# Kernel optimization log

Hardware: AMD Instinct MI355X
Metric: run time of the kernel (lower is better)

Reference implementation:

```python
import jax, jax.numpy as jnp
import numpy as np

# STBLISModule forward. Original torch code materializes kron(s_wav, t_wav)
# [K*J, N*T, N*T] and contracts: filtered[b,c,d,nt] = sum_k kron[d,nt,k] x[b,c,k].
# Since kron(S_p, T_q)[n*T+t, m*T+u] = S_p[n,m] * T_q[t,u] (row-major flatten),
# this equals the separable form y[b,c,p,q] = S_p @ X[b,c] @ T_q^T, which we
# compute directly (identical math, no giant dense kron matrix).

B, C, N, T = 4, 4, 512, 256
K, J = 4, 4


def setup_inputs() -> dict:
    key = jax.random.key(0)
    k1, k2, k3 = jax.random.split(key, 3)
    x = jax.random.normal(k1, (B, C, N, T), dtype=jnp.float32)
    s_wav = jax.random.normal(k2, (K, N, N), dtype=jnp.float32)  # spatial wavelet bank
    t_wav = jax.random.normal(k3, (J, T, T), dtype=jnp.float32)  # temporal wavelet bank
    return {"x": x, "s_wav": s_wav, "t_wav": t_wav}


def reference(x, s_wav, t_wav):
    # spatial filtering: [B,C,K,N,T]
    tmp = jnp.einsum('pnm,bcmu->bcpnu', s_wav, x)
    # temporal filtering: [B,C,K,J,N,T]; note sum over last axis u of t_wav
    # matches kron/einsum 'ijk,mlk' contraction (i.e. X @ T_q^T)
    y = jnp.einsum('bcpnu,qtu->bcpqnt', tmp, t_wav)
    b, c, p, q, n, t = y.shape
    # D index ordering d = p*J + q matches torch.kron filter ordering
    y = y.reshape(b, c * p * q, n, t)
    # dual ReLU split, concatenated on channel dim
    return jnp.concatenate([jax.nn.relu(y), jax.nn.relu(-y)], axis=1)
```

## Files before the change

kernel.cpp:

```cpp
#include <hip/hip_runtime.h>
#include <hip/hip_bf16.h>

typedef __attribute__((ext_vector_type(8))) short bf16x8;
typedef __attribute__((ext_vector_type(4))) float f32x4;
typedef __attribute__((ext_vector_type(4))) int   i32x4;
typedef __attribute__((ext_vector_type(2))) int   i32x2;

#define DEV static __device__ __forceinline__

DEV unsigned short f2bf(float f) {
  __hip_bfloat16 h = __float2bfloat16(f);
  return __builtin_bit_cast(unsigned short, h);
}
DEV int pack2(float a, float b) {
  return (int)f2bf(a) | ((int)f2bf(b) << 16);
}
DEV bf16x8 ldsFrag(const char* p, int off) {
  i32x4 v = *(const i32x4*)(p + off);
  return __builtin_bit_cast(bf16x8, v);
}


__global__ __launch_bounds__(256) void cvt_all(
    const float* __restrict__ x, unsigned short* __restrict__ xt,
    const float* __restrict__ sw, unsigned short* __restrict__ swb,
    const float* __restrict__ tw, unsigned short* __restrict__ twb)
{
  const int bid = blockIdx.x;
  const int tid = threadIdx.x;
  if (bid < 512) {
    __shared__ unsigned short lt[64][72];
    const int ut = bid & 3;
    const int mt = (bid >> 2) & 7;
    const int bc = bid >> 5;
    const int ul = tid & 63;
    const int mr = tid >> 6;
    const float* px = x + ((size_t)bc * 512 + mt * 64) * 256 + ut * 64;
#pragma unroll
    for (int r = 0; r < 16; r++) {
      int m = r * 4 + mr;
      lt[m][ul] = f2bf(px[(size_t)m * 256 + ul]);
    }
    __syncthreads();
    const int t8 = tid >> 5;
    const int a  = t8 & 3;
    const int bb = t8 >> 2;
    const int l0 = tid & 31;
    unsigned short* tilep =
        xt + (((size_t)(bc * 16 + ut * 4 + a)) * 16 + (mt * 2 + bb)) * 512;
#pragma unroll
    for (int h = 0; h < 2; h++) {
      int l = l0 + h * 32;
      int ur = a * 16 + (l & 15);
      int mb = bb * 32 + (l >> 4) * 8;
      i32x4 w;
#pragma unroll
      for (int j = 0; j < 4; j++)
        w[j] = (int)lt[mb + 2 * j][ur] | ((int)lt[mb + 2 * j + 1][ur] << 16);
      *(i32x4*)(tilep + l * 8) = w;
    }
  } else if (bid < 1024) {
    const int tile = (bid - 512) * 4 + (tid >> 6);
    const int l = tid & 63;
    const int mt2 = tile & 15;
    const int nt2 = (tile >> 4) & 31;
    const int p   = tile >> 9;
    const float* ps = sw + ((size_t)p * 512 + nt2 * 16 + (l & 15)) * 512
                         + mt2 * 32 + (l >> 4) * 8;
    f32x4 A = ((const f32x4*)ps)[0], Bv = ((const f32x4*)ps)[1];
    i32x4 w;
    w[0] = pack2(A[0], A[1]);  w[1] = pack2(A[2], A[3]);
    w[2] = pack2(Bv[0], Bv[1]); w[3] = pack2(Bv[2], Bv[3]);
    *(i32x4*)(swb + (size_t)tile * 512 + l * 8) = w;
  } else {
    const int tile = (bid - 1024) * 4 + (tid >> 6);
    const int l = tid & 63;
    const int ut2 = tile & 7;
    const int tt2 = (tile >> 3) & 15;
    const int q   = tile >> 7;
    const float* pt = tw + ((size_t)q * 256 + tt2 * 16 + (l & 15)) * 256
                         + ut2 * 32 + (l >> 4) * 8;
    f32x4 A = ((const f32x4*)pt)[0], Bv = ((const f32x4*)pt)[1];
    i32x4 w;
    w[0] = pack2(A[0], A[1]);  w[1] = pack2(A[2], A[3]);
    w[2] = pack2(Bv[0], Bv[1]); w[3] = pack2(Bv[2], Bv[3]);
    *(i32x4*)(twb + (size_t)tile * 512 + l * 8) = w;
  }
}

__global__ __launch_bounds__(512, 4) void stblis_main(
    const unsigned short* __restrict__ xt, const unsigned short* __restrict__ swb,
    const unsigned short* __restrict__ twb, float* __restrict__ out)
{
  __shared__ __align__(16) char lds[65536];
  char* const tmp = lds;
  char* const stg = lds + 32768;

  const int tid  = threadIdx.x;
  const int lane = tid & 63;
  const int wid  = tid >> 6;
  const int l15  = lane & 15;
  const int l4   = lane >> 4;

  const int bx = blockIdx.x;
  const int nt = bx & 7;
  const int p  = (bx >> 3) & 3;
  const int bc = bx >> 5;
  const int n0 = nt * 64;
  const int b = bc >> 2, c = bc & 3;

  const int wu = wid >> 1;
  const int wn = wid & 1;

  f32x4 acc[4][2];
#pragma unroll
  for (int i = 0; i < 4; i++)
#pragma unroll
    for (int j = 0; j < 2; j++) acc[i][j] = {0.f, 0.f, 0.f, 0.f};

  const unsigned short* xA = xt  + (((size_t)(bc * 16 + wu * 4)) * 16) * 512 + lane * 8;
  const unsigned short* sB = swb + (((size_t)(p * 32 + nt * 4 + wn * 2)) * 16) * 512 + lane * 8;

  for (int kc = 0; kc < 8; kc++) {
#pragma unroll
    for (int ks = 0; ks < 2; ks++) {
      const int mt2 = kc * 2 + ks;
      bf16x8 af[4], bg[2];
#pragma unroll
      for (int uf = 0; uf < 4; uf++)
        af[uf] = *(const bf16x8*)(xA + ((size_t)uf * 16 + mt2) * 512);
#pragma unroll
      for (int nf = 0; nf < 2; nf++)
        bg[nf] = *(const bf16x8*)(sB + ((size_t)nf * 16 + mt2) * 512);
#pragma unroll
      for (int uf = 0; uf < 4; uf++)
#pragma unroll
        for (int nf = 0; nf < 2; nf++)
          acc[uf][nf] = __builtin_amdgcn_mfma_f32_16x16x32_bf16(
              af[uf], bg[nf], acc[uf][nf], 0, 0, 0);
    }
  }

#pragma unroll
  for (int uf = 0; uf < 4; uf++)
#pragma unroll
    for (int nf = 0; nf < 2; nf++) {
      int u0 = wu * 64 + uf * 16 + l4 * 4;
      int n  = wn * 32 + nf * 16 + l15;
      i32x2 w;
      w[0] = pack2(acc[uf][nf][0], acc[uf][nf][1]);
      w[1] = pack2(acc[uf][nf][2], acc[uf][nf][3]);
      *(i32x2*)(tmp + n * 512 + (((u0 >> 3) ^ (n & 7)) << 4) + (u0 & 7) * 2) = w;
    }
  __syncthreads();

  const int tq = wid >> 1;
  const int nh = wid & 1;
  const int rowA = nh * 32 + l15;
  const int rowB = nh * 32 + 16 + l15;

  bf16x8 bgA[8], bgB[8];

#define LOADBG(dst, ph16)                                                      \
  {                                                                            \
    const int q_ = (ph16) >> 2, tc_ = (ph16) & 3;                              \
    const unsigned short* tA_ =                                                \
        twb + (((size_t)(q_ * 16 + tc_ * 4 + tq)) * 8) * 512 + lane * 8;       \
    _Pragma("unroll")                                                          \
    for (int us_ = 0; us_ < 8; us_++)                                          \
      dst[us_] = *(const bf16x8*)(tA_ + (size_t)us_ * 512);                    \
  }

#define SUB(cur, tcl)                                                          \
  {                                                                            \
    f32x4 a20 = {0.f, 0.f, 0.f, 0.f};                                          \
    f32x4 a21 = {0.f, 0.f, 0.f, 0.f};                                          \
    _Pragma("unroll")                                                          \
    for (int us_ = 0; us_ < 8; us_++) {                                        \
      const int slot_ = (us_ * 4 + l4) ^ (l15 & 7);                            \
      bf16x8 af0_ = ldsFrag(tmp, rowA * 512 + (slot_ << 4));                   \
      bf16x8 af1_ = ldsFrag(tmp, rowB * 512 + (slot_ << 4));                   \
      a20 = __builtin_amdgcn_mfma_f32_16x16x32_bf16(cur[us_], af0_, a20, 0, 0, 0); \
      a21 = __builtin_amdgcn_mfma_f32_16x16x32_bf16(cur[us_], af1_, a21, 0, 0, 0); \
    }                                                                          \
    const int c32_ = (tcl) * 16 + tq * 4 + l4;                                 \
    *(f32x4*)(stg + rowA * 512 + ((c32_ ^ (rowA & 15)) << 4)) = a20;           \
    *(f32x4*)(stg + rowB * 512 + ((c32_ ^ (rowB & 15)) << 4)) = a21;           \
  }

  LOADBG(bgA, 0);

  for (int ph = 0; ph < 8; ph++) {
    const int q  = ph >> 1;
    const int th = ph & 1;

    if (ph) asm volatile("s_barrier" ::: "memory");

    LOADBG(bgB, 2 * ph + 1);
    SUB(bgA, 0);
    if (ph < 7) LOADBG(bgA, 2 * ph + 2);
    SUB(bgB, 1);

    asm volatile("s_waitcnt lgkmcnt(0)\n\ts_barrier" ::: "memory");

    float* outQP = out + ((size_t)(b * 128 + c * 16 + p * 4 + q) * 512 + n0) * 256;
    float* outQN = outQP + (size_t)64 * 512 * 256;
#pragma unroll
    for (int it = 0; it < 4; it++) {
      int g   = it * 512 + tid;
      int r   = g >> 5;
      int c32 = g & 31;
      f32x4 y = *(const f32x4*)(stg + r * 512 + ((c32 ^ (r & 15)) << 4));
      f32x4 vP, vN;
#pragma unroll
      for (int j = 0; j < 4; j++) {
        vP[j] = fmaxf(y[j], 0.f);
        vN[j] = fmaxf(-y[j], 0.f);
      }
      size_t go = (size_t)r * 256 + th * 128 + c32 * 4;
      *(f32x4*)(outQP + go) = vP;
      *(f32x4*)(outQN + go) = vN;
    }
  }
#undef SUB
#undef LOADBG
}

extern "C" void kernel_launch(void* const* d_in, const int* in_sizes, int n_in,
                              void* d_out, int out_size, void* d_ws, size_t ws_size,
                              hipStream_t stream) {
  (void)in_sizes; (void)n_in; (void)out_size; (void)ws_size;
  const float* x  = (const float*)d_in[0];
  const float* sw = (const float*)d_in[1];
  const float* tw = (const float*)d_in[2];
  float* out = (float*)d_out;

  unsigned short* xt  = (unsigned short*)d_ws;
  unsigned short* swb = xt + (size_t)16 * 16 * 16 * 512;
  unsigned short* twb = swb + (size_t)2048 * 512;

  cvt_all<<<dim3(1152), dim3(256), 0, stream>>>(x, xt, sw, swb, tw, twb);
  stblis_main<<<dim3(512), dim3(512), 0, stream>>>(xt, swb, twb, out);
}
```

Before: 74.17 us.

## Process two spatial tiles per block, overlapping second stage-1 GEMM with first stage-2

```diff
diff --git a/kernel.cpp b/kernel.cpp
--- a/kernel.cpp
+++ b/kernel.cpp
@@ -88,13 +88,14 @@
   }
 }
 
-__global__ __launch_bounds__(512, 4) void stblis_main(
+__global__ __launch_bounds__(512, 2) void stblis_main(
     const unsigned short* __restrict__ xt, const unsigned short* __restrict__ swb,
     const unsigned short* __restrict__ twb, float* __restrict__ out)
 {
-  __shared__ __align__(16) char lds[65536];
-  char* const tmp = lds;
-  char* const stg = lds + 32768;
+  __shared__ __align__(16) char lds[131072];
+  char* const tmp0 = lds;
+  char* const tmp1 = lds + 32768;
+  char* const stgb = lds + 65536;
 
   const int tid  = threadIdx.x;
   const int lane = tid & 63;
@@ -102,24 +103,25 @@
   const int l15  = lane & 15;
   const int l4   = lane >> 4;
 
-  const int bx = blockIdx.x;
-  const int nt = bx & 7;
-  const int p  = (bx >> 3) & 3;
-  const int bc = bx >> 5;
-  const int n0 = nt * 64;
+  const int bx  = blockIdx.x;
+  const int ntp = bx & 3;
+  const int p   = (bx >> 2) & 3;
+  const int bc  = bx >> 4;
+  const int nt0 = ntp * 2, nt1 = ntp * 2 + 1;
   const int b = bc >> 2, c = bc & 3;
 
   const int wu = wid >> 1;
   const int wn = wid & 1;
 
+  const unsigned short* xA  = xt  + (((size_t)(bc * 16 + wu * 4)) * 16) * 512 + lane * 8;
+  const unsigned short* sB0 = swb + (((size_t)(p * 32 + nt0 * 4 + wn * 2)) * 16) * 512 + lane * 8;
+  const unsigned short* sB1 = swb + (((size_t)(p * 32 + nt1 * 4 + wn * 2)) * 16) * 512 + lane * 8;
+
   f32x4 acc[4][2];
 #pragma unroll
   for (int i = 0; i < 4; i++)
 #pragma unroll
     for (int j = 0; j < 2; j++) acc[i][j] = {0.f, 0.f, 0.f, 0.f};
-
-  const unsigned short* xA = xt  + (((size_t)(bc * 16 + wu * 4)) * 16) * 512 + lane * 8;
-  const unsigned short* sB = swb + (((size_t)(p * 32 + nt * 4 + wn * 2)) * 16) * 512 + lane * 8;
 
   for (int kc = 0; kc < 8; kc++) {
 #pragma unroll
@@ -131,7 +133,7 @@
         af[uf] = *(const bf16x8*)(xA + ((size_t)uf * 16 + mt2) * 512);
 #pragma unroll
       for (int nf = 0; nf < 2; nf++)
-        bg[nf] = *(const bf16x8*)(sB + ((size_t)nf * 16 + mt2) * 512);
+        bg[nf] = *(const bf16x8*)(sB0 + ((size_t)nf * 16 + mt2) * 512);
 #pragma unroll
       for (int uf = 0; uf < 4; uf++)
 #pragma unroll
@@ -140,7 +142,6 @@
               af[uf], bg[nf], acc[uf][nf], 0, 0, 0);
     }
   }
-
 #pragma unroll
   for (int uf = 0; uf < 4; uf++)
 #pragma unroll
@@ -150,14 +151,17 @@
       i32x2 w;
       w[0] = pack2(acc[uf][nf][0], acc[uf][nf][1]);
       w[1] = pack2(acc[uf][nf][2], acc[uf][nf][3]);
-      *(i32x2*)(tmp + n * 512 + (((u0 >> 3) ^ (n & 7)) << 4) + (u0 & 7) * 2) = w;
+      *(i32x2*)(tmp0 + n * 512 + (((u0 >> 3) ^ (n & 7)) << 4) + (u0 & 7) * 2) = w;
     }
   __syncthreads();
 
   const int tq = wid >> 1;
   const int nh = wid & 1;
   const int rowA = nh * 32 + l15;
-  const int rowB = nh * 32 + 16 + l15;
+  const int rowB = rowA + 16;
+
+  float* const outB0 = out + (((size_t)(b * 128 + c * 16 + p * 4)) * 512 + nt0 * 64) * 256;
+  float* const outB1 = out + (((size_t)(b * 128 + c * 16 + p * 4)) * 512 + nt1 * 64) * 256;
 
   bf16x8 bgA[8], bgB[8];
 
@@ -171,59 +175,125 @@
       dst[us_] = *(const bf16x8*)(tA_ + (size_t)us_ * 512);                    \
   }
 
-#define SUB(cur, tcl)                                                          \
+#define SUB(tmpP, stgP, cur, tcl)                                              \
   {                                                                            \
     f32x4 a20 = {0.f, 0.f, 0.f, 0.f};                                          \
     f32x4 a21 = {0.f, 0.f, 0.f, 0.f};                                          \
     _Pragma("unroll")                                                          \
     for (int us_ = 0; us_ < 8; us_++) {                                        \
       const int slot_ = (us_ * 4 + l4) ^ (l15 & 7);                            \
-      bf16x8 af0_ = ldsFrag(tmp, rowA * 512 + (slot_ << 4));                   \
-      bf16x8 af1_ = ldsFrag(tmp, rowB * 512 + (slot_ << 4));                   \
+      bf16x8 af0_ = ldsFrag(tmpP, rowA * 512 + (slot_ << 4));                  \
+      bf16x8 af1_ = ldsFrag(tmpP, rowB * 512 + (slot_ << 4));                  \
       a20 = __builtin_amdgcn_mfma_f32_16x16x32_bf16(cur[us_], af0_, a20, 0, 0, 0); \
       a21 = __builtin_amdgcn_mfma_f32_16x16x32_bf16(cur[us_], af1_, a21, 0, 0, 0); \
     }                                                                          \
     const int c32_ = (tcl) * 16 + tq * 4 + l4;                                 \
-    *(f32x4*)(stg + rowA * 512 + ((c32_ ^ (rowA & 15)) << 4)) = a20;           \
-    *(f32x4*)(stg + rowB * 512 + ((c32_ ^ (rowB & 15)) << 4)) = a21;           \
-  }
+    *(f32x4*)(stgP + rowA * 512 + ((c32_ ^ (rowA & 15)) << 4)) = a20;          \
+    *(f32x4*)(stgP + rowB * 512 + ((c32_ ^ (rowB & 15)) << 4)) = a21;          \
+  }
+
+#define STOREPH(stgR, outBase, qv, thv)                                        \
+  {                                                                            \
+    float* oP_ = (outBase) + (size_t)(qv) * 131072;                            \
+    float* oN_ = oP_ + 8388608;                                                \
+    _Pragma("unroll")                                                          \
+    for (int it_ = 0; it_ < 4; it_++) {                                        \
+      int g_ = it_ * 512 + tid;                                                \
+      int r_ = g_ >> 5;                                                        \
+      int c32_ = g_ & 31;                                                      \
+      f32x4 y_ = *(const f32x4*)(stgR + r_ * 512 + ((c32_ ^ (r_ & 15)) << 4)); \
+      f32x4 vP_, vN_;                                                          \
+      _Pragma("unroll")                                                        \
+      for (int j_ = 0; j_ < 4; j_++) {                                         \
+        vP_[j_] = fmaxf(y_[j_], 0.f);                                          \
+        vN_[j_] = fmaxf(-y_[j_], 0.f);                                         \
+      }                                                                        \
+      size_t go_ = (size_t)r_ * 256 + (thv) * 128 + c32_ * 4;                  \
+      *(f32x4*)(oP_ + go_) = vP_;                                              \
+      *(f32x4*)(oN_ + go_) = vN_;                                              \
+    }                                                                          \
+  }
+
+#define LOADA1(K, F0, F1, F2, F3, G0, G1)                                      \
+  {                                                                            \
+    const int mt2_ = (K);                                                      \
+    F0 = *(const bf16x8*)(xA + ((size_t)0 * 16 + mt2_) * 512);                 \
+    F1 = *(const bf16x8*)(xA + ((size_t)1 * 16 + mt2_) * 512);                 \
+    F2 = *(const bf16x8*)(xA + ((size_t)2 * 16 + mt2_) * 512);                 \
+    F3 = *(const bf16x8*)(xA + ((size_t)3 * 16 + mt2_) * 512);                 \
+    G0 = *(const bf16x8*)(sB1 + ((size_t)0 * 16 + mt2_) * 512);                \
+    G1 = *(const bf16x8*)(sB1 + ((size_t)1 * 16 + mt2_) * 512);                \
+  }
+
+#define MFMA1K(F0, F1, F2, F3, G0, G1)                                         \
+  c1_00 = __builtin_amdgcn_mfma_f32_16x16x32_bf16(F0, G0, c1_00, 0, 0, 0);     \
+  c1_01 = __builtin_amdgcn_mfma_f32_16x16x32_bf16(F0, G1, c1_01, 0, 0, 0);     \
+  c1_10 = __builtin_amdgcn_mfma_f32_16x16x32_bf16(F1, G0, c1_10, 0, 0, 0);     \
+  c1_11 = __builtin_amdgcn_mfma_f32_16x16x32_bf16(F1, G1, c1_11, 0, 0, 0);     \
+  c1_20 = __builtin_amdgcn_mfma_f32_16x16x32_bf16(F2, G0, c1_20, 0, 0, 0);     \
+  c1_21 = __builtin_amdgcn_mfma_f32_16x16x32_bf16(F2, G1, c1_21, 0, 0, 0);     \
+  c1_30 = __builtin_amdgcn_mfma_f32_16x16x32_bf16(F3, G0, c1_30, 0, 0, 0);     \
+  c1_31 = __builtin_amdgcn_mfma_f32_16x16x32_bf16(F3, G1, c1_31, 0, 0, 0);
+
+#define WT1(ACC, UF, NF)                                                       \
+  {                                                                            \
+    int u0_ = wu * 64 + (UF) * 16 + l4 * 4;                                    \
+    int n_  = wn * 32 + (NF) * 16 + l15;                                       \
+    i32x2 w_;                                                                  \
+    w_[0] = pack2(ACC[0], ACC[1]);                                             \
+    w_[1] = pack2(ACC[2], ACC[3]);                                             \
+    *(i32x2*)(tmp1 + n_ * 512 + (((u0_ >> 3) ^ (n_ & 7)) << 4) + (u0_ & 7) * 2) = w_; \
+  }
+
+  f32x4 c1_00 = {0.f,0.f,0.f,0.f}, c1_01 = {0.f,0.f,0.f,0.f};
+  f32x4 c1_10 = {0.f,0.f,0.f,0.f}, c1_11 = {0.f,0.f,0.f,0.f};
+  f32x4 c1_20 = {0.f,0.f,0.f,0.f}, c1_21 = {0.f,0.f,0.f,0.f};
+  f32x4 c1_30 = {0.f,0.f,0.f,0.f}, c1_31 = {0.f,0.f,0.f,0.f};
+  bf16x8 k0f0, k0f1, k0f2, k0f3, k0g0, k0g1;
+  bf16x8 k1f0, k1f1, k1f2, k1f3, k1g0, k1g1;
 
   LOADBG(bgA, 0);
 
   for (int ph = 0; ph < 8; ph++) {
-    const int q  = ph >> 1;
-    const int th = ph & 1;
-
-    if (ph) asm volatile("s_barrier" ::: "memory");
+    char* stgW = stgb + (ph & 1) * 32768;
+    LOADA1(2 * ph,     k0f0, k0f1, k0f2, k0f3, k0g0, k0g1);
+    LOADA1(2 * ph + 1, k1f0, k1f1, k1f2, k1f3, k1g0, k1g1);
 
     LOADBG(bgB, 2 * ph + 1);
-    SUB(bgA, 0);
+    SUB(tmp0, stgW, bgA, 0);
     if (ph < 7) LOADBG(bgA, 2 * ph + 2);
-    SUB(bgB, 1);
+    SUB(tmp0, stgW, bgB, 1);
+
+    MFMA1K(k0f0, k0f1, k0f2, k0f3, k0g0, k0g1);
+    MFMA1K(k1f0, k1f1, k1f2, k1f3, k1g0, k1g1);
 
     asm volatile("s_waitcnt lgkmcnt(0)\n\ts_barrier" ::: "memory");
-
-    float* outQP = out + ((size_t)(b * 128 + c * 16 + p * 4 + q) * 512 + n0) * 256;
-    float* outQN = outQP + (size_t)64 * 512 * 256;
-#pragma unroll
-    for (int it = 0; it < 4; it++) {
-      int g   = it * 512 + tid;
-      int r   = g >> 5;
-      int c32 = g & 31;
-      f32x4 y = *(const f32x4*)(stg + r * 512 + ((c32 ^ (r & 15)) << 4));
-      f32x4 vP, vN;
-#pragma unroll
-      for (int j = 0; j < 4; j++) {
-        vP[j] = fmaxf(y[j], 0.f);
-        vN[j] = fmaxf(-y[j], 0.f);
-      }
-      size_t go = (size_t)r * 256 + th * 128 + c32 * 4;
-      *(f32x4*)(outQP + go) = vP;
-      *(f32x4*)(outQN + go) = vN;
-    }
-  }
+    STOREPH(stgW, outB0, ph >> 1, ph & 1);
+  }
+
+  LOADBG(bgA, 0);
+  WT1(c1_00, 0, 0) WT1(c1_01, 0, 1)
+  WT1(c1_10, 1, 0) WT1(c1_11, 1, 1)
+  WT1(c1_20, 2, 0) WT1(c1_21, 2, 1)
+  WT1(c1_30, 3, 0) WT1(c1_31, 3, 1)
+  asm volatile("s_waitcnt lgkmcnt(0)\n\ts_barrier" ::: "memory");
+
+  for (int ph = 0; ph < 8; ph++) {
+    char* stgW = stgb + (ph & 1) * 32768;
+    LOADBG(bgB, 2 * ph + 1);
+    SUB(tmp1, stgW, bgA, 0);
+    if (ph < 7) LOADBG(bgA, 2 * ph + 2);
+    SUB(tmp1, stgW, bgB, 1);
+    asm volatile("s_waitcnt lgkmcnt(0)\n\ts_barrier" ::: "memory");
+    STOREPH(stgW, outB1, ph >> 1, ph & 1);
+  }
+
+#undef LOADBG
 #undef SUB
-#undef LOADBG
+#undef STOREPH
+#undef LOADA1
+#undef MFMA1K
+#undef WT1
 }
 
 extern "C" void kernel_launch(void* const* d_in, const int* in_sizes, int n_in,
@@ -240,5 +310,5 @@
   unsigned short* twb = swb + (size_t)2048 * 512;
 
   cvt_all<<<dim3(1152), dim3(256), 0, stream>>>(x, xt, sw, swb, tw, twb);
-  stblis_main<<<dim3(512), dim3(512), 0, stream>>>(xt, swb, twb, out);
-}
+  stblis_main<<<dim3(256), dim3(512), 0, stream>>>(xt, swb, twb, out);
+}
```

Measured after the change: 78.53 us. 1.06x slower.
